# Performance work log

Measured on AMD Instinct MI355X. Metric: run time of the kernel, lower is better.

## Reference

```python
import jax, jax.numpy as jnp
import numpy as np

EPS = 1e-06

def _feature_map(x):
    # elu(x) + 1 -> strictly positive feature map
    return jax.nn.elu(x) + 1.0

def setup_inputs() -> dict:
    key = jax.random.key(0)
    kq, kk, kv = jax.random.split(key, 3)
    B, H, N, D = 1, 16, 2048, 64
    Q = jax.random.normal(kq, (B, H, N, D), dtype=jnp.float32)
    K = jax.random.normal(kk, (B, H, N, D), dtype=jnp.float32)
    V = jax.random.normal(kv, (B, H, N, D), dtype=jnp.float32)
    return {"Q": Q, "K": K, "V": V, "causal": 1}

def reference(Q, K, V, causal):
    Qf = _feature_map(Q)  # (B,H,N,D)
    Kf = _feature_map(K)  # (B,H,N,D)
    if causal:
        # prefix sums of per-position outer products K_m V_m^T  -> (B,H,N,D,Dv)
        KV_prefix = jnp.cumsum(Kf[..., :, None] * V[..., None, :], axis=2)
        Kf_prefix = jnp.cumsum(Kf, axis=2)  # (B,H,N,D)
        num = jnp.einsum('bhnd,bhnde->bhne', Qf, KV_prefix)
        den = jnp.einsum('bhnd,bhnd->bhn', Qf, Kf_prefix)[..., None]
        return num / (den + EPS)
    else:
        KV = jnp.einsum('bhnd,bhne->bhde', Kf, V)            # (B,H,D,Dv)
        num = jnp.einsum('bhnd,bhde->bhne', Qf, KV)          # (B,H,N,Dv)
        den = jnp.einsum('bhnd,bhd->bhn', Qf, Kf.sum(axis=2))[..., None]
        return num / (den + EPS)
```

## Files before the change

kernel.cpp:

```cpp
#include <hip/hip_runtime.h>

#define Hh   16
#define Nn   2048
#define Dd   64
#define DVv  64
#define Ll   64
#define Cc   (Nn / Ll)
#define HCc  (Hh * Cc)
#define CS   (65 * 64)
#define EPSf 1e-6f
#define LDP  72

typedef __attribute__((ext_vector_type(8))) __bf16 bf16x8;
typedef __attribute__((ext_vector_type(4))) __bf16 bf16x4;
typedef __attribute__((ext_vector_type(4))) float  f32x4;

__device__ __forceinline__ float fmap(float x) {
    return x > 0.0f ? (x + 1.0f) : __expf(x);
}
__device__ __forceinline__ __bf16 tobf(float x) { return (__bf16)x; }

__global__ __launch_bounds__(256) void k_chunk_sums(
    const float* __restrict__ Kg, const float* __restrict__ Vg,
    __bf16* __restrict__ Sws, __bf16* __restrict__ Kfb,
    __bf16* __restrict__ Vtb)
{
    __shared__ __align__(16) __bf16 sKT[Dd][LDP];
    __shared__ __align__(16) __bf16 sVT[80][LDP];
    const int t  = threadIdx.x;
    const int hc = blockIdx.x;
    const float4* K4 = (const float4*)(Kg + (size_t)hc * (Ll * Dd));
    const float4* V4 = (const float4*)(Vg + (size_t)hc * (Ll * DVv));
    __bf16* Kfo = Kfb + (size_t)hc * (Ll * Dd);
    for (int i = t; i < (Ll * Dd) / 4; i += 256) {
        float4 k4 = K4[i];
        float4 v4 = V4[i];
        const int m  = i >> 4;
        const int c0 = (i & 15) * 4;
        bf16x4 kv = { tobf(fmap(k4.x)), tobf(fmap(k4.y)), tobf(fmap(k4.z)), tobf(fmap(k4.w)) };
        sKT[c0 + 0][m] = kv[0];
        sKT[c0 + 1][m] = kv[1];
        sKT[c0 + 2][m] = kv[2];
        sKT[c0 + 3][m] = kv[3];
        *(bf16x4*)&Kfo[m * Dd + c0] = kv;
        sVT[c0 + 0][m] = tobf(v4.x);
        sVT[c0 + 1][m] = tobf(v4.y);
        sVT[c0 + 2][m] = tobf(v4.z);
        sVT[c0 + 3][m] = tobf(v4.w);
    }
    for (int i = t; i < 16 * LDP; i += 256) {
        const int r = i / LDP, c = i % LDP;
        sVT[64 + r][c] = (r == 0) ? (__bf16)1.0f : (__bf16)0.0f;
    }
    __syncthreads();

    const int lane = t & 63, wv = t >> 6;
    const int col = lane & 15, quad = lane >> 4;
    __bf16* So = Sws + (size_t)hc * CS;
    for (int et = 0; et < 5; ++et) {
        f32x4 acc = {0.f, 0.f, 0.f, 0.f};
#pragma unroll
        for (int ks = 0; ks < 2; ++ks) {
            bf16x8 a = *(const bf16x8*)&sKT[wv * 16 + col][ks * 32 + quad * 8];
            bf16x8 b = *(const bf16x8*)&sVT[et * 16 + col][ks * 32 + quad * 8];
            acc = __builtin_amdgcn_mfma_f32_16x16x32_bf16(a, b, acc, 0, 0, 0);
        }
        bf16x4 s4 = { tobf(acc[0]), tobf(acc[1]), tobf(acc[2]), tobf(acc[3]) };
        const int d = wv * 16 + quad * 4;
        if (et < 4) {
            *(bf16x4*)&So[(et * 16 + col) * Dd + d] = s4;
        } else if (col == 0) {
            *(bf16x4*)&So[64 * Dd + d] = s4;
        }
    }
    __bf16* Vto = Vtb + (size_t)hc * (Ll * DVv);
    for (int i = t; i < (Ll * DVv) / 8; i += 256) {
        const int e = i >> 3, m0 = (i & 7) * 8;
        *(bf16x8*)&Vto[e * Ll + m0] = *(const bf16x8*)&sVT[e][m0];
    }
}

__global__ __launch_bounds__(256) void k_prefix(__bf16* __restrict__ Sws)
{
    const int gid = blockIdx.x * 256 + threadIdx.x;
    if (gid >= Hh * (CS / 8)) return;
    const int h  = gid / (CS / 8);
    const int sl = gid % (CS / 8);
    __bf16* base = Sws + (size_t)h * Cc * CS + sl * 8;
    float run[8];
#pragma unroll
    for (int j = 0; j < 8; ++j) run[j] = 0.0f;
#pragma unroll
    for (int cb = 0; cb < 4; ++cb) {
        bf16x8 v[8];
#pragma unroll
        for (int k = 0; k < 8; ++k)
            v[k] = *(const bf16x8*)(base + (size_t)(cb * 8 + k) * CS);
#pragma unroll
        for (int k = 0; k < 8; ++k) {
            bf16x8 o;
#pragma unroll
            for (int j = 0; j < 8; ++j) {
                o[j] = tobf(run[j]);
                run[j] += (float)v[k][j];
            }
            *(bf16x8*)(base + (size_t)(cb * 8 + k) * CS) = o;
        }
    }
}

__global__ __launch_bounds__(256) void k_output(
    const float* __restrict__ Qg, const __bf16* __restrict__ Kfb,
    const __bf16* __restrict__ Vtb, const __bf16* __restrict__ Sws,
    float* __restrict__ Og)
{
    __shared__ __align__(16) __bf16 aQ[Ll][LDP];
    __shared__ __align__(16) __bf16 aK[Ll][LDP];
    __shared__ __align__(16) __bf16 sW[Ll][LDP];
    __shared__ __align__(16) __bf16 bV[80][LDP];
    __shared__ __align__(16) __bf16 bS[80][LDP];
    const int t  = threadIdx.x;
    const int hc = blockIdx.x;
    const int lane = t & 63, wv = t >> 6;
    const int col = lane & 15, quad = lane >> 4;

    {
        const float4* Q4 = (const float4*)(Qg + (size_t)hc * (Ll * Dd));
        for (int i = t; i < (Ll * Dd) / 4; i += 256) {
            float4 q4 = Q4[i];
            const int m  = i >> 4;
            const int c0 = (i & 15) * 4;
            bf16x4 qv = { tobf(fmap(q4.x)), tobf(fmap(q4.y)), tobf(fmap(q4.z)), tobf(fmap(q4.w)) };
            *(bf16x4*)&aQ[m][c0] = qv;
        }
    }
    {
        const __bf16* Kfo = Kfb + (size_t)hc * (Ll * Dd);
        const __bf16* Vto = Vtb + (size_t)hc * (Ll * DVv);
        const __bf16* Sp  = Sws + (size_t)hc * CS;
        for (int i = t; i < (Ll * Dd) / 8; i += 256) {
            const int r = i >> 3, c0 = (i & 7) * 8;
            *(bf16x8*)&aK[r][c0] = *(const bf16x8*)(Kfo + i * 8);
            *(bf16x8*)&bV[r][c0] = *(const bf16x8*)(Vto + i * 8);
        }
        for (int i = t; i < CS / 8; i += 256) {
            const int r = i >> 3, c0 = (i & 7) * 8;
            *(bf16x8*)&bS[r][c0] = *(const bf16x8*)(Sp + i * 8);
        }
        for (int i = t; i < 16 * LDP; i += 256) {
            const int r = i / LDP, cc = i % LDP;
            bV[64 + r][cc] = (r == 0) ? (__bf16)1.0f : (__bf16)0.0f;
            if (r > 0) bS[64 + r][cc] = (__bf16)0.0f;
        }
    }
    __syncthreads();

#pragma unroll 1
    for (int mt = 0; mt < 4; ++mt) {
        f32x4 wacc = {0.f, 0.f, 0.f, 0.f};
#pragma unroll
        for (int ks = 0; ks < 2; ++ks) {
            bf16x8 a = *(const bf16x8*)&aQ[wv * 16 + col][ks * 32 + quad * 8];
            bf16x8 b = *(const bf16x8*)&aK[mt * 16 + col][ks * 32 + quad * 8];
            wacc = __builtin_amdgcn_mfma_f32_16x16x32_bf16(a, b, wacc, 0, 0, 0);
        }
#pragma unroll
        for (int j = 0; j < 4; ++j) {
            const int n = wv * 16 + quad * 4 + j;
            const int m = mt * 16 + col;
            sW[n][m] = tobf(m <= n ? wacc[j] : 0.0f);
        }
    }
    __syncthreads();

    f32x4 accs[5];
#pragma unroll 1
    for (int et = 0; et < 5; ++et) {
        f32x4 acc = {0.f, 0.f, 0.f, 0.f};
#pragma unroll
        for (int ks = 0; ks < 2; ++ks) {
            bf16x8 a = *(const bf16x8*)&sW[wv * 16 + col][ks * 32 + quad * 8];
            bf16x8 b = *(const bf16x8*)&bV[et * 16 + col][ks * 32 + quad * 8];
            acc = __builtin_amdgcn_mfma_f32_16x16x32_bf16(a, b, acc, 0, 0, 0);
        }
#pragma unroll
        for (int ks = 0; ks < 2; ++ks) {
            bf16x8 a = *(const bf16x8*)&aQ[wv * 16 + col][ks * 32 + quad * 8];
            bf16x8 b = *(const bf16x8*)&bS[et * 16 + col][ks * 32 + quad * 8];
            acc = __builtin_amdgcn_mfma_f32_16x16x32_bf16(a, b, acc, 0, 0, 0);
        }
        accs[et] = acc;
    }
    float dn[4];
#pragma unroll
    for (int j = 0; j < 4; ++j) dn[j] = __shfl(accs[4][j], lane & 48);

    float* Oc = Og + (size_t)hc * (Ll * DVv);
#pragma unroll
    for (int et = 0; et < 4; ++et) {
#pragma unroll
        for (int j = 0; j < 4; ++j) {
            const int n = wv * 16 + quad * 4 + j;
            Oc[n * DVv + et * 16 + col] = accs[et][j] / (dn[j] + EPSf);
        }
    }
}

extern "C" void kernel_launch(void* const* d_in, const int* in_sizes, int n_in,
                              void* d_out, int out_size, void* d_ws, size_t ws_size,
                              hipStream_t stream) {
    const float* Q = (const float*)d_in[0];
    const float* K = (const float*)d_in[1];
    const float* V = (const float*)d_in[2];
    unsigned char* ws = (unsigned char*)d_ws;
    __bf16* Sws = (__bf16*)ws;
    __bf16* Kfb = (__bf16*)(ws + (size_t)HCc * CS * 2);
    __bf16* Vtb = Kfb + (size_t)HCc * Ll * Dd;
    float* out = (float*)d_out;

    k_chunk_sums<<<HCc, 256, 0, stream>>>(K, V, Sws, Kfb, Vtb);
    k_prefix<<<(Hh * (CS / 8) + 255) / 256, 256, 0, stream>>>(Sws);
    k_output<<<HCc, 256, 0, stream>>>(Q, Kfb, Vtb, Sws, out);
}
```

Measured before the change: 89.66 us.

## Fuse chunk-state prefix scan into output kernel, dropping separate prefix launch

Removes the separate prefix-sum kernel. Each output block now sums the chunk states of all earlier chunks for its head straight from global memory into shared memory. This saves one kernel launch and the in-place write-back of the prefix states. In exchange, the prefix work is repeated, so total global reads grow roughly quadratically with the chunk index, with late chunks reading up to 31 chunk states, and blocks become load-imbalanced.

```diff
diff --git a/kernel.cpp b/kernel.cpp
--- a/kernel.cpp
+++ b/kernel.cpp
@@ -80,35 +80,6 @@
     }
 }
 
-__global__ __launch_bounds__(256) void k_prefix(__bf16* __restrict__ Sws)
-{
-    const int gid = blockIdx.x * 256 + threadIdx.x;
-    if (gid >= Hh * (CS / 8)) return;
-    const int h  = gid / (CS / 8);
-    const int sl = gid % (CS / 8);
-    __bf16* base = Sws + (size_t)h * Cc * CS + sl * 8;
-    float run[8];
-#pragma unroll
-    for (int j = 0; j < 8; ++j) run[j] = 0.0f;
-#pragma unroll
-    for (int cb = 0; cb < 4; ++cb) {
-        bf16x8 v[8];
-#pragma unroll
-        for (int k = 0; k < 8; ++k)
-            v[k] = *(const bf16x8*)(base + (size_t)(cb * 8 + k) * CS);
-#pragma unroll
-        for (int k = 0; k < 8; ++k) {
-            bf16x8 o;
-#pragma unroll
-            for (int j = 0; j < 8; ++j) {
-                o[j] = tobf(run[j]);
-                run[j] += (float)v[k][j];
-            }
-            *(bf16x8*)(base + (size_t)(cb * 8 + k) * CS) = o;
-        }
-    }
-}
-
 __global__ __launch_bounds__(256) void k_output(
     const float* __restrict__ Qg, const __bf16* __restrict__ Kfb,
     const __bf16* __restrict__ Vtb, const __bf16* __restrict__ Sws,
@@ -121,8 +92,37 @@
     __shared__ __align__(16) __bf16 bS[80][LDP];
     const int t  = threadIdx.x;
     const int hc = blockIdx.x;
+    const int h  = hc >> 5, c = hc & 31;
     const int lane = t & 63, wv = t >> 6;
     const int col = lane & 15, quad = lane >> 4;
+
+    {
+        const __bf16* Sh = Sws + (size_t)h * Cc * CS;
+        const int nb = (c + 7) >> 3;
+        for (int sl = t; sl < CS / 8; sl += 256) {
+            float run[8];
+#pragma unroll
+            for (int j = 0; j < 8; ++j) run[j] = 0.0f;
+            for (int cb = 0; cb < nb; ++cb) {
+                bf16x8 v[8];
+#pragma unroll
+                for (int k = 0; k < 8; ++k)
+                    v[k] = *(const bf16x8*)(Sh + (size_t)(cb * 8 + k) * CS + sl * 8);
+#pragma unroll
+                for (int k = 0; k < 8; ++k) {
+                    if (cb * 8 + k < c) {
+#pragma unroll
+                        for (int j = 0; j < 8; ++j) run[j] += (float)v[k][j];
+                    }
+                }
+            }
+            bf16x8 o;
+#pragma unroll
+            for (int j = 0; j < 8; ++j) o[j] = tobf(run[j]);
+            const int e = sl >> 3, d0 = (sl & 7) * 8;
+            *(bf16x8*)&bS[e][d0] = o;
+        }
+    }
 
     {
         const float4* Q4 = (const float4*)(Qg + (size_t)hc * (Ll * Dd));
@@ -133,19 +133,12 @@
             bf16x4 qv = { tobf(fmap(q4.x)), tobf(fmap(q4.y)), tobf(fmap(q4.z)), tobf(fmap(q4.w)) };
             *(bf16x4*)&aQ[m][c0] = qv;
         }
-    }
-    {
         const __bf16* Kfo = Kfb + (size_t)hc * (Ll * Dd);
         const __bf16* Vto = Vtb + (size_t)hc * (Ll * DVv);
-        const __bf16* Sp  = Sws + (size_t)hc * CS;
         for (int i = t; i < (Ll * Dd) / 8; i += 256) {
             const int r = i >> 3, c0 = (i & 7) * 8;
             *(bf16x8*)&aK[r][c0] = *(const bf16x8*)(Kfo + i * 8);
             *(bf16x8*)&bV[r][c0] = *(const bf16x8*)(Vto + i * 8);
-        }
-        for (int i = t; i < CS / 8; i += 256) {
-            const int r = i >> 3, c0 = (i & 7) * 8;
-            *(bf16x8*)&bS[r][c0] = *(const bf16x8*)(Sp + i * 8);
         }
         for (int i = t; i < 16 * LDP; i += 256) {
             const int r = i / LDP, cc = i % LDP;
@@ -219,6 +212,5 @@
     float* out = (float*)d_out;
 
     k_chunk_sums<<<HCc, 256, 0, stream>>>(K, V, Sws, Kfb, Vtb);
-    k_prefix<<<(Hh * (CS / 8) + 255) / 256, 256, 0, stream>>>(Sws);
     k_output<<<HCc, 256, 0, stream>>>(Q, Kfb, Vtb, Sws, out);
 }
```

After: 91.78 us. 2.4% more time.
